# Optimization experiments

Measured on AMD Instinct MI355X. Metric: run time of the kernel, lower is better.

Reference implementation:

```python
import math
import jax, jax.numpy as jnp
from jax import lax
import numpy as np

B, S, D = 4, 128, 256          # batch, image side (l_max = S*S), d_model
FO = 64                        # filter_order (MLP width)
EMB = 3                        # emb_dim (time + 1 band sine/cosine)
FAST, SLOW, TARGET = 0.3, 1.5, 0.01


def setup_inputs() -> dict:
    key = jax.random.key(0)
    ks = jax.random.split(key, 20)
    d3 = 3 * D
    def rn(k, shp, scale):
        return jax.random.normal(k, shp, jnp.float32) * scale
    inp = {
        "x": jax.random.normal(ks[0], (B, S * S, D), jnp.float32),
        # in_proj / out_proj
        "in_w": rn(ks[1], (D, d3), 1.0 / math.sqrt(D)),
        "in_b": jnp.zeros((d3,), jnp.float32),
        "out_w": rn(ks[2], (D, D), 1.0 / math.sqrt(D)),
        "out_b": jnp.zeros((D,), jnp.float32),
        # depthwise 3x3 short filter
        "sf_w": rn(ks[3], (d3, 1, 3, 3), 1.0 / 3.0),
        "sf_b": jnp.zeros((d3,), jnp.float32),
        # Sin activation frequency (shared across all Sin uses; w=1, train_freq=True)
        "freq": jnp.ones((1, FO), jnp.float32),
        # X implicit filter MLP: Linear(3,FO) -> Sin -> Linear(FO,FO) -> Sin -> Linear(FO,FO) -> Sin -> Linear(FO,D,no bias)
        "xw0": rn(ks[4], (EMB, FO), 0.5), "xb0": jnp.zeros((FO,), jnp.float32),
        "xw1": rn(ks[5], (FO, FO), 1.0 / math.sqrt(FO)), "xb1": jnp.zeros((FO,), jnp.float32),
        "xw2": rn(ks[6], (FO, FO), 1.0 / math.sqrt(FO)), "xb2": jnp.zeros((FO,), jnp.float32),
        "xw3": rn(ks[7], (FO, D), 1.0 / math.sqrt(FO)),
        # Y implicit filter MLP (same structure)
        "yw0": rn(ks[8], (EMB, FO), 0.5), "yb0": jnp.zeros((FO,), jnp.float32),
        "yw1": rn(ks[9], (FO, FO), 1.0 / math.sqrt(FO)), "yb1": jnp.zeros((FO,), jnp.float32),
        "yw2": rn(ks[10], (FO, FO), 1.0 / math.sqrt(FO)), "yb2": jnp.zeros((FO,), jnp.float32),
        "yw3": rn(ks[11], (FO, D), 1.0 / math.sqrt(FO)),
        # HyenaFilter2d residual bias D (torch: randn)
        "fbias": jax.random.normal(ks[12], (D,), jnp.float32),
    }
    return inp


def _pos_emb():
    # PositionalEmbedding with emb_dim=3 -> bands=1
    t = jnp.linspace(0.0, 1.0, S)[None, :, None]                 # (1,S,1)
    tr = jnp.linspace(0.0, S - 1.0, S)[None, :, None]
    w_ang = 2.0 * math.pi * tr / S
    f = jnp.linspace(1e-4, 0.0, 1)[None, None]                   # bands=1
    zc = jnp.exp(-1j * f * w_ang)                                # (1,S,1) complex
    z = jnp.concatenate([t, zc.real, zc.imag], axis=-1)          # (1,S,3)
    return z.astype(jnp.float32), t.astype(jnp.float32)


def _decay(t):
    max_d = math.log(TARGET) / FAST
    min_d = math.log(TARGET) / SLOW
    deltas = jnp.linspace(min_d, max_d, D)[None, None]           # (1,1,D) buffer
    return jnp.exp(-t * jnp.abs(deltas))                         # (1,S,D)


def _mlp(z, freq, w0, b0, w1, b1, w2, b2, w3):
    h = jnp.sin(freq * (z @ w0 + b0))
    h = jnp.sin(freq * (h @ w1 + b1))
    h = jnp.sin(freq * (h @ w2 + b2))
    return h @ w3                                                # (1,S,D)


def _fftconv2d(u, k, Db):
    # u: (B,D,S,S), k: (D,S,S), Db: (D,)
    n = 2 * S
    kf = jnp.fft.rfft2(k.astype(jnp.float32), s=(n, n)) / n
    uf = jnp.fft.rfft2(u.astype(jnp.float32), s=(n, n))
    y = jnp.fft.irfft2(uf * kf, s=(n, n))[..., :S, :S]
    return y + u * Db[None, :, None, None]


def reference(x, in_w, in_b, out_w, out_b, sf_w, sf_b, freq,
              xw0, xb0, xw1, xb1, xw2, xb2, xw3,
              yw0, yb0, yw1, yb1, yw2, yb2, yw3, fbias):
    d3 = 3 * D
    # projection and reshape to 2D grid: b (h w) c -> b c h w
    u = x @ in_w + in_b                                          # (B,L,3D)
    u = u.reshape(B, S, S, d3).transpose(0, 3, 1, 2)             # (B,3D,S,S)
    # depthwise 3x3 short filter, padding=2, crop to S (matches Conv padding=2 + [:S])
    uc = lax.conv_general_dilated(u, sf_w, (1, 1), ((2, 2), (2, 2)),
                                  feature_group_count=d3,
                                  dimension_numbers=("NCHW", "OIHW", "NCHW"))
    uc = uc[..., :S, :S] + sf_b[None, :, None, None]
    x0, x1, v = jnp.split(uc, 3, axis=1)                         # each (B,D,S,S)
    # implicit separable 2D filter
    z, t = _pos_emb()
    dec = _decay(t)
    hx = _mlp(z, freq, xw0, xb0, xw1, xb1, xw2, xb2, xw3) * dec  # (1,S,D)
    hy = _mlp(z, freq, yw0, yb0, yw1, yb1, yw2, yb2, yw3) * dec
    k = jnp.einsum('ijk,imk->ijmk', hx, hy)[0]                   # (S,S,D)
    k = jnp.transpose(k, (2, 0, 1))                              # (D,S,S)
    # hyena recurrence (order=2): single gated fft conv
    v = v * x1
    v = _fftconv2d(v, k, fbias)
    y = v * x0
    y = y.transpose(0, 2, 3, 1).reshape(B, S * S, D)             # b c h w -> b (h w) c
    return y @ out_w + out_b
```

## Files before the change

kernel.cpp:

```cpp
#include <hip/hip_runtime.h>
#include <hip/hip_bf16.h>

#define S_DIM 128
#define B_DIM 4
#define L_DIM (S_DIM * S_DIM)

typedef __bf16 bf16x8 __attribute__((ext_vector_type(8)));
typedef float f32x4 __attribute__((ext_vector_type(4)));

__device__ __forceinline__ float b2f(unsigned short u) {
    union { unsigned int i; float f; } v;
    v.i = ((unsigned int)u) << 16;
    return v.f;
}
__device__ __forceinline__ unsigned short f2b(float f) {
    union { float f; unsigned int i; } v;
    v.f = f;
    unsigned int x = v.i;
    return (unsigned short)((x + 0x7FFFu + ((x >> 16) & 1u)) >> 16);
}
__device__ __forceinline__ float ldx(const void* p, size_t i, int f32) {
    return f32 ? ((const float*)p)[i] : b2f(((const unsigned short*)p)[i]);
}

__global__ __launch_bounds__(256) void sniff_dtype(const unsigned short* __restrict__ x,
                                                   int* __restrict__ flag) {
    __shared__ int cnt;
    if (threadIdx.x == 0) cnt = 0;
    __syncthreads();
    int c = 0;
    for (int i = threadIdx.x; i < 32768; i += 256) {
        unsigned int e = (x[i] >> 7) & 0xFFu;
        if (e >= 0x91u) c++;
    }
    atomicAdd(&cnt, c);
    __syncthreads();
    if (threadIdx.x == 0) flag[0] = (cnt > 64) ? 1 : 0;
}

__global__ void transpose_any(const void* __restrict__ src,
                              unsigned short* __restrict__ dst, int R, int C,
                              const int* __restrict__ flag) {
    const int f = flag[0];
    int idx = blockIdx.x * 256 + threadIdx.x;
    if (idx >= R * C) return;
    int r = idx / C, c = idx - r * C;
    dst[c * R + r] = f2b(ldx(src, idx, f));
}

__global__ __launch_bounds__(256) void filter_mlp(
    const void* __restrict__ freq,
    const void* __restrict__ w0, const void* __restrict__ b0,
    const void* __restrict__ w1, const void* __restrict__ b1,
    const void* __restrict__ w2, const void* __restrict__ b2,
    const void* __restrict__ w3,
    float* __restrict__ out, const int* __restrict__ flag)
{
    __shared__ float hs[64], gs[64];
    const int f32f = flag[0];
    const int s   = blockIdx.x;
    const int tid = threadIdx.x;
    const float t = (float)s / (float)(S_DIM - 1);
    const float ang = 1e-4f * 2.0f * 3.14159265358979323846f * ((float)s / (float)S_DIM);
    const float z0 = t, z1 = cosf(ang), z2 = -sinf(ang);

    if (tid < 64) {
        float fr = ldx(freq, tid, f32f);
        float a = z0 * ldx(w0, 0 * 64 + tid, f32f) + z1 * ldx(w0, 1 * 64 + tid, f32f) +
                  z2 * ldx(w0, 2 * 64 + tid, f32f) + ldx(b0, tid, f32f);
        hs[tid] = sinf(fr * a);
    }
    __syncthreads();
    if (tid < 64) {
        float fr = ldx(freq, tid, f32f);
        float a = ldx(b1, tid, f32f);
        for (int e = 0; e < 64; e++) a += hs[e] * ldx(w1, e * 64 + tid, f32f);
        gs[tid] = sinf(fr * a);
    }
    __syncthreads();
    if (tid < 64) {
        float fr = ldx(freq, tid, f32f);
        float a = ldx(b2, tid, f32f);
        for (int e = 0; e < 64; e++) a += gs[e] * ldx(w2, e * 64 + tid, f32f);
        hs[tid] = sinf(fr * a);
    }
    __syncthreads();
    {
        const float min_d = -3.0701134573253943f;
        const float max_d = -15.350567286626971f;
        float a = 0.f;
        for (int e = 0; e < 64; e++) a += hs[e] * ldx(w3, e * 256 + tid, f32f);
        float delta = min_d + (max_d - min_d) * ((float)tid / 255.0f);
        float dec = expf(-t * fabsf(delta));
        out[s * 256 + tid] = a * dec;
    }
}

__global__ __launch_bounds__(256) void gemm_bt(
    const void* __restrict__ A, size_t a_off, int a_ext,
    const unsigned short* __restrict__ BT,
    const void* __restrict__ bias, int bias_ext,
    void* __restrict__ C, size_t c_off, int c_ext,
    int M, int N, int K, const int* __restrict__ flag)
{
    __shared__ unsigned short As[128 * 40];
    __shared__ unsigned short Bs[128 * 40];

    const int f     = flag[0];
    const int a_f32 = a_ext && f;
    const int b_f32 = bias_ext && f;
    const int c_f32 = c_ext && f;

    const int tid  = threadIdx.x;
    const int m0   = blockIdx.x * 128;
    const int n0   = blockIdx.y * 128;
    const int wid  = tid >> 6;
    const int lane = tid & 63;
    const int lrow = lane & 15;
    const int quad = lane >> 4;
    const int wr   = wid >> 1, wc = wid & 1;

    f32x4 acc[4][4];
#pragma unroll
    for (int a = 0; a < 4; a++)
#pragma unroll
        for (int b = 0; b < 4; b++)
#pragma unroll
            for (int r = 0; r < 4; r++) acc[a][b][r] = 0.0f;

    for (int kc = 0; kc < K; kc += 32) {
#pragma unroll
        for (int h = 0; h < 2; h++) {
            int c    = tid + h * 256;
            int row  = c >> 2;
            int col8 = (c & 3) * 8;
            size_t aidx = a_off + (size_t)(m0 + row) * K + kc + col8;
            if (a_f32) {
                const float4* ga = (const float4*)((const float*)A + aidx);
                float4 p0 = ga[0], p1 = ga[1];
                uint4 w;
                w.x = (unsigned int)f2b(p0.x) | ((unsigned int)f2b(p0.y) << 16);
                w.y = (unsigned int)f2b(p0.z) | ((unsigned int)f2b(p0.w) << 16);
                w.z = (unsigned int)f2b(p1.x) | ((unsigned int)f2b(p1.y) << 16);
                w.w = (unsigned int)f2b(p1.z) | ((unsigned int)f2b(p1.w) << 16);
                *(uint4*)(&As[row * 40 + col8]) = w;
            } else {
                *(uint4*)(&As[row * 40 + col8]) =
                    *(const uint4*)((const unsigned short*)A + aidx);
            }
            *(uint4*)(&Bs[row * 40 + col8]) =
                *(const uint4*)(BT + (size_t)(n0 + row) * K + kc + col8);
        }
        __syncthreads();

        bf16x8 af[4], bfr[4];
#pragma unroll
        for (int fm = 0; fm < 4; fm++)
            af[fm] = *(const bf16x8*)(&As[(wr * 64 + fm * 16 + lrow) * 40 + quad * 8]);
#pragma unroll
        for (int fn = 0; fn < 4; fn++)
            bfr[fn] = *(const bf16x8*)(&Bs[(wc * 64 + fn * 16 + lrow) * 40 + quad * 8]);
#pragma unroll
        for (int fm = 0; fm < 4; fm++)
#pragma unroll
            for (int fn = 0; fn < 4; fn++)
                acc[fm][fn] = __builtin_amdgcn_mfma_f32_16x16x32_bf16(
                    af[fm], bfr[fn], acc[fm][fn], 0, 0, 0);
        __syncthreads();
    }

#pragma unroll
    for (int fm = 0; fm < 4; fm++) {
#pragma unroll
        for (int fn = 0; fn < 4; fn++) {
            int gcol = n0 + wc * 64 + fn * 16 + lrow;
            float bv = ldx(bias, gcol, b_f32);
#pragma unroll
            for (int r = 0; r < 4; r++) {
                int grow = m0 + wr * 64 + fm * 16 + quad * 4 + r;
                size_t cidx = c_off + (size_t)grow * N + gcol;
                float val = acc[fm][fn][r] + bv;
                if (c_f32) ((float*)C)[cidx] = val;
                else       ((unsigned short*)C)[cidx] = f2b(val);
            }
        }
    }
}

__global__ __launch_bounds__(192) void conv3_gate(
    const unsigned short* __restrict__ U, size_t u_zs,
    const void* __restrict__ sfw, const void* __restrict__ sfb,
    unsigned short* __restrict__ Wb, unsigned short* __restrict__ X0, size_t o_zs,
    const int* __restrict__ flag)
{
    __shared__ __align__(16) float x1f[2][256];

    const int f32f = flag[0];
    const int i    = blockIdx.x;
    const int j0   = blockIdx.y * 32;
    const int tid  = threadIdx.x;
    const int wv   = tid >> 6;
    const int lane = tid & 63;
    const int ch0  = wv * 256 + lane * 4;

    const unsigned short* Ub = U + (size_t)blockIdx.z * u_zs;
    unsigned short* Wbb = Wb + (size_t)blockIdx.z * o_zs;
    unsigned short* X0b = X0 + (size_t)blockIdx.z * o_zs;

    float wgt[3][3][4], bias[4];
#pragma unroll
    for (int c = 0; c < 4; c++) {
        int ch = ch0 + c;
        bias[c] = ldx(sfb, ch, f32f);
#pragma unroll
        for (int ki = 0; ki < 3; ki++)
#pragma unroll
            for (int kj = 0; kj < 3; kj++)
                wgt[ki][kj][c] = ldx(sfw, ch * 9 + ki * 3 + kj, f32f);
    }

    bool rok[3];
    const unsigned short* rp[3];
#pragma unroll
    for (int ki = 0; ki < 3; ki++) {
        int row = i + ki - 2;
        rok[ki] = (row >= 0);
        rp[ki]  = Ub + (size_t)(row * S_DIM) * 768 + ch0;
    }

    float win[3][3][4];
#define DLOAD(slot, col)                                                       \
    { _Pragma("unroll") for (int ki = 0; ki < 3; ki++) {                       \
        if (rok[ki] && (col) >= 0) {                                           \
            uint2 p = *(const uint2*)(rp[ki] + (size_t)(col) * 768);           \
            win[slot][ki][0] = b2f((unsigned short)p.x);                       \
            win[slot][ki][1] = b2f((unsigned short)(p.x >> 16));               \
            win[slot][ki][2] = b2f((unsigned short)p.y);                       \
            win[slot][ki][3] = b2f((unsigned short)(p.y >> 16));               \
        } else {                                                               \
            win[slot][ki][0] = 0.f; win[slot][ki][1] = 0.f;                    \
            win[slot][ki][2] = 0.f; win[slot][ki][3] = 0.f;                    \
        } } }

    DLOAD(0, j0 - 2)
    DLOAD(1, j0 - 1)

    uint2 nxt[3];
#pragma unroll
    for (int ki = 0; ki < 3; ki++) {
        uint2 p; p.x = 0u; p.y = 0u;
        if (rok[ki]) p = *(const uint2*)(rp[ki] + (size_t)j0 * 768);
        nxt[ki] = p;
    }

#pragma unroll
    for (int jj = 0; jj < 32; jj++) {
        const int j  = j0 + jj;
        const int sA = jj % 3, sB = (jj + 1) % 3, sC = (jj + 2) % 3;

#pragma unroll
        for (int ki = 0; ki < 3; ki++) {
            win[sC][ki][0] = b2f((unsigned short)nxt[ki].x);
            win[sC][ki][1] = b2f((unsigned short)(nxt[ki].x >> 16));
            win[sC][ki][2] = b2f((unsigned short)nxt[ki].y);
            win[sC][ki][3] = b2f((unsigned short)(nxt[ki].y >> 16));
        }
        {
            const int jn = j + 1;
            const bool jok = (jn < S_DIM);
#pragma unroll
            for (int ki = 0; ki < 3; ki++) {
                uint2 p; p.x = 0u; p.y = 0u;
                if (jok && rok[ki]) p = *(const uint2*)(rp[ki] + (size_t)jn * 768);
                nxt[ki] = p;
            }
        }

        float o[4];
#pragma unroll
        for (int c = 0; c < 4; c++) {
            float a = bias[c];
#pragma unroll
            for (int ki = 0; ki < 3; ki++)
                a += wgt[ki][0][c] * win[sA][ki][c]
                   + wgt[ki][1][c] * win[sB][ki][c]
                   + wgt[ki][2][c] * win[sC][ki][c];
            o[c] = a;
        }

        const size_t oidx = (size_t)(i * S_DIM + j) * 256 + lane * 4;
        if (wv == 1) {
            float4 v4; v4.x = o[0]; v4.y = o[1]; v4.z = o[2]; v4.w = o[3];
            *(float4*)(&x1f[jj & 1][lane * 4]) = v4;
        } else if (wv == 0) {
            unsigned int lo = (unsigned int)f2b(o[0]) | ((unsigned int)f2b(o[1]) << 16);
            unsigned int hi = (unsigned int)f2b(o[2]) | ((unsigned int)f2b(o[3]) << 16);
            uint2 st; st.x = lo; st.y = hi;
            *(uint2*)(&X0b[oidx]) = st;
        }
        __syncthreads();
        if (wv == 2) {
            float4 xp = *(const float4*)(&x1f[jj & 1][lane * 4]);
            float r0 = o[0] * xp.x;
            float r1 = o[1] * xp.y;
            float r2 = o[2] * xp.z;
            float r3 = o[3] * xp.w;
            unsigned int lo = (unsigned int)f2b(r0) | ((unsigned int)f2b(r1) << 16);
            unsigned int hi = (unsigned int)f2b(r2) | ((unsigned int)f2b(r3) << 16);
            uint2 st; st.x = lo; st.y = hi;
            *(uint2*)(&Wbb[oidx]) = st;
        }
    }
#undef DLOAD
}

__global__ __launch_bounds__(256) void conv_j(
    const unsigned short* __restrict__ Wb, size_t zs,
    const float* __restrict__ hy,
    unsigned short* __restrict__ Aout)
{
    __shared__ unsigned short wl[S_DIM * 256];
    const int i = blockIdx.x;
    const int h = blockIdx.y;
    const int tid = threadIdx.x;
    const size_t zoff = (size_t)blockIdx.z * zs;
    const size_t sbase = zoff + (size_t)(i * S_DIM) * 256;

    const uint4* gsrc = (const uint4*)(Wb + sbase);
    for (int c = tid; c < 4096; c += 256) ((uint4*)wl)[c] = gsrc[c];
    __syncthreads();

    const int d = tid;
    for (int pick = 0; pick < 2; pick++) {
        const int jt = pick ? (7 - h) : h;
        const int j0 = jt * 16;
        float acc[16];
#pragma unroll
        for (int jj = 0; jj < 16; jj++) acc[jj] = 0.f;

        float Wn[19];
#pragma unroll
        for (int t = 0; t < 19; t++) {
            int r = j0 - 3 + t;
            Wn[t] = (r >= 0) ? b2f(wl[r * 256 + d]) : 0.f;
        }
        const int qmax = j0 + 15;
        for (int q0 = 0; q0 <= qmax; q0 += 4) {
            float hv[4];
#pragma unroll
            for (int idx = 0; idx < 4; idx++) hv[idx] = hy[(q0 + idx) * 256 + d];
#pragma unroll
            for (int idx = 0; idx < 4; idx++)
#pragma unroll
                for (int jj = 0; jj < 16; jj++)
                    acc[jj] += hv[idx] * Wn[jj + 3 - idx];
            if (q0 + 4 <= qmax) {
#pragma unroll
                for (int t = 18; t >= 4; t--) Wn[t] = Wn[t - 4];
#pragma unroll
                for (int t = 0; t < 4; t++) {
                    int r = j0 - q0 - 7 + t;
                    Wn[t] = (r >= 0) ? b2f(wl[r * 256 + d]) : 0.f;
                }
            }
        }
#pragma unroll
        for (int jj = 0; jj < 16; jj++)
            Aout[sbase + (size_t)(j0 + jj) * 256 + d] = f2b(acc[jj]);
    }
}

__global__ __launch_bounds__(256) void conv_i(
    const unsigned short* __restrict__ Ain, size_t zs,
    const float* __restrict__ hx,
    const unsigned short* __restrict__ Wb,
    const unsigned short* __restrict__ X0,
    const void* __restrict__ fbias,
    unsigned short* __restrict__ Gout,
    const int* __restrict__ flag)
{
    __shared__ unsigned short al[S_DIM * 256];
    const int f32f = flag[0];
    const int j = blockIdx.x;
    const int h = blockIdx.y;
    const int tid = threadIdx.x;
    const size_t zoff = (size_t)blockIdx.z * zs;

    for (int c = tid; c < 4096; c += 256) {
        int row = c >> 5;
        int off = c & 31;
        const uint4* gsrc = (const uint4*)(Ain + zoff + (size_t)(row * S_DIM + j) * 256) + off;
        ((uint4*)al)[c] = *gsrc;
    }
    __syncthreads();

    const int d = tid;
    const float fb = ldx(fbias, d, f32f);
    for (int pick = 0; pick < 2; pick++) {
        const int it = pick ? (7 - h) : h;
        const int i0 = it * 16;
        float acc[16];
#pragma unroll
        for (int ii = 0; ii < 16; ii++) acc[ii] = 0.f;

        float Wn[19];
#pragma unroll
        for (int t = 0; t < 19; t++) {
            int r = i0 - 3 + t;
            Wn[t] = (r >= 0) ? b2f(al[r * 256 + d]) : 0.f;
        }
        const int qmax = i0 + 15;
        for (int q0 = 0; q0 <= qmax; q0 += 4) {
            float hv[4];
#pragma unroll
            for (int idx = 0; idx < 4; idx++) hv[idx] = hx[(q0 + idx) * 256 + d];
#pragma unroll
            for (int idx = 0; idx < 4; idx++)
#pragma unroll
                for (int ii = 0; ii < 16; ii++)
                    acc[ii] += hv[idx] * Wn[ii + 3 - idx];
            if (q0 + 4 <= qmax) {
#pragma unroll
                for (int t = 18; t >= 4; t--) Wn[t] = Wn[t - 4];
#pragma unroll
                for (int t = 0; t < 4; t++) {
                    int r = i0 - q0 - 7 + t;
                    Wn[t] = (r >= 0) ? b2f(al[r * 256 + d]) : 0.f;
                }
            }
        }
#pragma unroll
        for (int ii = 0; ii < 16; ii++) {
            int i = i0 + ii;
            size_t idx = zoff + (size_t)(i * S_DIM + j) * 256 + d;
            float wv  = b2f(Wb[idx]);
            float x0v = b2f(X0[idx]);
            float y = acc[ii] * (1.0f / 256.0f) + wv * fb;
            Gout[idx] = f2b(y * x0v);
        }
    }
}

extern "C" void kernel_launch(void* const* d_in, const int* in_sizes, int n_in,
                              void* d_out, int out_size, void* d_ws, size_t ws_size,
                              hipStream_t stream)
{
    const void* x     = d_in[0];
    const void* in_w  = d_in[1];
    const void* in_b  = d_in[2];
    const void* out_w = d_in[3];
    const void* out_b_= d_in[4];
    const void* sf_w  = d_in[5];
    const void* sf_b  = d_in[6];
    const void* freq  = d_in[7];
    const void* xw0 = d_in[8];  const void* xb0 = d_in[9];
    const void* xw1 = d_in[10]; const void* xb1 = d_in[11];
    const void* xw2 = d_in[12]; const void* xb2 = d_in[13];
    const void* xw3 = d_in[14];
    const void* yw0 = d_in[15]; const void* yb0 = d_in[16];
    const void* yw1 = d_in[17]; const void* yb1 = d_in[18];
    const void* yw2 = d_in[19]; const void* yb2 = d_in[20];
    const void* yw3 = d_in[21];
    const void* fbias = d_in[22];

    char* ws = (char*)d_ws;
    const size_t UZ  = (size_t)L_DIM * 768;
    const size_t OZ  = (size_t)L_DIM * 256;

    const size_t need_fused = 168558608;
    bool fused = (ws_size >= need_fused);

    if (fused) {
        unsigned short* u_f  = (unsigned short*)(ws + 0);
        unsigned short* A_f  = (unsigned short*)(ws + 0);
        unsigned short* G_f  = (unsigned short*)(ws + 33554432);
        unsigned short* Wb_f = (unsigned short*)(ws + 100663296);
        unsigned short* X0_f = (unsigned short*)(ws + 134217728);
        float* hx            = (float*)(ws + 167772160);
        float* hy            = (float*)(ws + 167903232);
        unsigned short* tin  = (unsigned short*)(ws + 168034304);
        unsigned short* tout = (unsigned short*)(ws + 168427520);
        int* flag            = (int*)(ws + 168558592);

        sniff_dtype<<<1, 256, 0, stream>>>((const unsigned short*)x, flag);
        transpose_any<<<dim3(768), 256, 0, stream>>>(in_w, tin, 256, 768, flag);
        transpose_any<<<dim3(256), 256, 0, stream>>>(out_w, tout, 256, 256, flag);
        filter_mlp<<<dim3(S_DIM), 256, 0, stream>>>(freq, xw0, xb0, xw1, xb1, xw2, xb2, xw3, hx, flag);
        filter_mlp<<<dim3(S_DIM), 256, 0, stream>>>(freq, yw0, yb0, yw1, yb1, yw2, yb2, yw3, hy, flag);

        gemm_bt<<<dim3(512, 6), 256, 0, stream>>>(
            x, 0, 1, tin, in_b, 1, u_f, 0, 0, B_DIM * L_DIM, 768, 256, flag);
        conv3_gate<<<dim3(S_DIM, 4, B_DIM), 192, 0, stream>>>(
            u_f, UZ, sf_w, sf_b, Wb_f, X0_f, OZ, flag);
        conv_j<<<dim3(S_DIM, 4, B_DIM), 256, 0, stream>>>(Wb_f, OZ, hy, A_f);
        conv_i<<<dim3(S_DIM, 4, B_DIM), 256, 0, stream>>>(
            A_f, OZ, hx, Wb_f, X0_f, fbias, G_f, flag);
        gemm_bt<<<dim3(512, 2), 256, 0, stream>>>(
            G_f, 0, 0, tout, out_b_, 1, d_out, 0, 1, B_DIM * L_DIM, 256, 256, flag);
    } else {
        unsigned short* u_b  = (unsigned short*)(ws + 0);
        unsigned short* A_b  = (unsigned short*)(ws + 0);
        unsigned short* G_b  = (unsigned short*)(ws + 8388608);
        unsigned short* Wb_b = (unsigned short*)(ws + 25165824);
        unsigned short* X0_b = (unsigned short*)(ws + 33554432);
        float* hx            = (float*)(ws + 41943040);
        float* hy            = (float*)(ws + 42074112);
        unsigned short* tin  = (unsigned short*)(ws + 42205184);
        unsigned short* tout = (unsigned short*)(ws + 42598400);
        int* flag            = (int*)(ws + 42729472);

        sniff_dtype<<<1, 256, 0, stream>>>((const unsigned short*)x, flag);
        transpose_any<<<dim3(768), 256, 0, stream>>>(in_w, tin, 256, 768, flag);
        transpose_any<<<dim3(256), 256, 0, stream>>>(out_w, tout, 256, 256, flag);
        filter_mlp<<<dim3(S_DIM), 256, 0, stream>>>(freq, xw0, xb0, xw1, xb1, xw2, xb2, xw3, hx, flag);
        filter_mlp<<<dim3(S_DIM), 256, 0, stream>>>(freq, yw0, yb0, yw1, yb1, yw2, yb2, yw3, hy, flag);

        for (int b = 0; b < B_DIM; b++) {
            size_t xoff = (size_t)b * OZ;
            gemm_bt<<<dim3(128, 6), 256, 0, stream>>>(
                x, xoff, 1, tin, in_b, 1, u_b, 0, 0, L_DIM, 768, 256, flag);
            conv3_gate<<<dim3(S_DIM, 4, 1), 192, 0, stream>>>(
                u_b, 0, sf_w, sf_b, Wb_b, X0_b, 0, flag);
            conv_j<<<dim3(S_DIM, 4, 1), 256, 0, stream>>>(Wb_b, 0, hy, A_b);
            conv_i<<<dim3(S_DIM, 4, 1), 256, 0, stream>>>(
                A_b, 0, hx, Wb_b, X0_b, fbias, G_b, flag);
            gemm_bt<<<dim3(128, 2), 256, 0, stream>>>(
                G_b, 0, 0, tout, out_b_, 1, d_out, xoff, 1, L_DIM, 256, 256, flag);
        }
    }
}
```

Before: 582.9 us.

## Fully unroll causal conv loops with ring-buffer window, one block per row, pre-cast x

The causal direct convolutions now have each block process all 8 output tiles of a row. The loops are fully unrolled and use a 20-slot register ring buffer indexed at compile time, which removes the per-step register shifting, and launch bounds request 2 blocks per CU. This cuts the grid fourfold so the shared-memory row is staged once instead of four times. A separate cast kernel converts x to bf16 before the input GEMM, so the GEMM reads bf16. The trade-offs are far fewer blocks (512) and lower parallelism for the conv kernels, a large unrolled code size, and an extra pass over x.

```diff
diff --git a/kernel.cpp b/kernel.cpp
--- a/kernel.cpp
+++ b/kernel.cpp
@@ -22,6 +22,8 @@
 __device__ __forceinline__ float ldx(const void* p, size_t i, int f32) {
     return f32 ? ((const float*)p)[i] : b2f(((const unsigned short*)p)[i]);
 }
+
+#define SLOT(r) ((((r) % 20) + 20) % 20)
 
 __global__ __launch_bounds__(256) void sniff_dtype(const unsigned short* __restrict__ x,
                                                    int* __restrict__ flag) {
@@ -46,6 +48,31 @@
     if (idx >= R * C) return;
     int r = idx / C, c = idx - r * C;
     dst[c * R + r] = f2b(ldx(src, idx, f));
+}
+
+__global__ __launch_bounds__(256) void cast_to_bf16(
+    const void* __restrict__ src, size_t s_off,
+    unsigned short* __restrict__ dst, size_t n,
+    const int* __restrict__ flag)
+{
+    const int f = flag[0];
+    size_t idx = ((size_t)blockIdx.x * 256 + threadIdx.x) * 8;
+    const size_t stride = (size_t)gridDim.x * 256 * 8;
+    for (; idx < n; idx += stride) {
+        if (f) {
+            const float4* s4 = (const float4*)((const float*)src + s_off + idx);
+            float4 a = s4[0], b = s4[1];
+            uint4 w;
+            w.x = (unsigned int)f2b(a.x) | ((unsigned int)f2b(a.y) << 16);
+            w.y = (unsigned int)f2b(a.z) | ((unsigned int)f2b(a.w) << 16);
+            w.z = (unsigned int)f2b(b.x) | ((unsigned int)f2b(b.y) << 16);
+            w.w = (unsigned int)f2b(b.z) | ((unsigned int)f2b(b.w) << 16);
+            *(uint4*)(dst + idx) = w;
+        } else {
+            *(uint4*)(dst + idx) =
+                *(const uint4*)((const unsigned short*)src + s_off + idx);
+        }
+    }
 }
 
 __global__ __launch_bounds__(256) void filter_mlp(
@@ -314,14 +341,13 @@
 #undef DLOAD
 }
 
-__global__ __launch_bounds__(256) void conv_j(
+__global__ __launch_bounds__(256, 2) void conv_j(
     const unsigned short* __restrict__ Wb, size_t zs,
     const float* __restrict__ hy,
     unsigned short* __restrict__ Aout)
 {
     __shared__ unsigned short wl[S_DIM * 256];
     const int i = blockIdx.x;
-    const int h = blockIdx.y;
     const int tid = threadIdx.x;
     const size_t zoff = (size_t)blockIdx.z * zs;
     const size_t sbase = zoff + (size_t)(i * S_DIM) * 256;
@@ -331,21 +357,24 @@
     __syncthreads();
 
     const int d = tid;
-    for (int pick = 0; pick < 2; pick++) {
-        const int jt = pick ? (7 - h) : h;
+    float win[20];
+
+#pragma unroll
+    for (int jt = 0; jt < 8; jt++) {
         const int j0 = jt * 16;
         float acc[16];
 #pragma unroll
         for (int jj = 0; jj < 16; jj++) acc[jj] = 0.f;
 
-        float Wn[19];
 #pragma unroll
         for (int t = 0; t < 19; t++) {
-            int r = j0 - 3 + t;
-            Wn[t] = (r >= 0) ? b2f(wl[r * 256 + d]) : 0.f;
-        }
-        const int qmax = j0 + 15;
-        for (int q0 = 0; q0 <= qmax; q0 += 4) {
+            const int r = j0 - 3 + t;
+            win[SLOT(r)] = (r >= 0) ? b2f(wl[r * 256 + d]) : 0.f;
+        }
+        const int nsteps = 4 * (jt + 1);
+#pragma unroll
+        for (int s = 0; s < nsteps; s++) {
+            const int q0 = 4 * s;
             float hv[4];
 #pragma unroll
             for (int idx = 0; idx < 4; idx++) hv[idx] = hy[(q0 + idx) * 256 + d];
@@ -353,14 +382,12 @@
             for (int idx = 0; idx < 4; idx++)
 #pragma unroll
                 for (int jj = 0; jj < 16; jj++)
-                    acc[jj] += hv[idx] * Wn[jj + 3 - idx];
-            if (q0 + 4 <= qmax) {
-#pragma unroll
-                for (int t = 18; t >= 4; t--) Wn[t] = Wn[t - 4];
+                    acc[jj] += hv[idx] * win[SLOT(j0 + jj - (q0 + idx))];
+            if (s + 1 < nsteps) {
 #pragma unroll
                 for (int t = 0; t < 4; t++) {
-                    int r = j0 - q0 - 7 + t;
-                    Wn[t] = (r >= 0) ? b2f(wl[r * 256 + d]) : 0.f;
+                    const int r = j0 - q0 - 7 + t;
+                    win[SLOT(r)] = (r >= 0) ? b2f(wl[r * 256 + d]) : 0.f;
                 }
             }
         }
@@ -370,7 +397,7 @@
     }
 }
 
-__global__ __launch_bounds__(256) void conv_i(
+__global__ __launch_bounds__(256, 2) void conv_i(
     const unsigned short* __restrict__ Ain, size_t zs,
     const float* __restrict__ hx,
     const unsigned short* __restrict__ Wb,
@@ -382,7 +409,6 @@
     __shared__ unsigned short al[S_DIM * 256];
     const int f32f = flag[0];
     const int j = blockIdx.x;
-    const int h = blockIdx.y;
     const int tid = threadIdx.x;
     const size_t zoff = (size_t)blockIdx.z * zs;
 
@@ -396,21 +422,24 @@
 
     const int d = tid;
     const float fb = ldx(fbias, d, f32f);
-    for (int pick = 0; pick < 2; pick++) {
-        const int it = pick ? (7 - h) : h;
+    float win[20];
+
+#pragma unroll
+    for (int it = 0; it < 8; it++) {
         const int i0 = it * 16;
         float acc[16];
 #pragma unroll
         for (int ii = 0; ii < 16; ii++) acc[ii] = 0.f;
 
-        float Wn[19];
 #pragma unroll
         for (int t = 0; t < 19; t++) {
-            int r = i0 - 3 + t;
-            Wn[t] = (r >= 0) ? b2f(al[r * 256 + d]) : 0.f;
-        }
-        const int qmax = i0 + 15;
-        for (int q0 = 0; q0 <= qmax; q0 += 4) {
+            const int r = i0 - 3 + t;
+            win[SLOT(r)] = (r >= 0) ? b2f(al[r * 256 + d]) : 0.f;
+        }
+        const int nsteps = 4 * (it + 1);
+#pragma unroll
+        for (int s = 0; s < nsteps; s++) {
+            const int q0 = 4 * s;
             float hv[4];
 #pragma unroll
             for (int idx = 0; idx < 4; idx++) hv[idx] = hx[(q0 + idx) * 256 + d];
@@ -418,14 +447,12 @@
             for (int idx = 0; idx < 4; idx++)
 #pragma unroll
                 for (int ii = 0; ii < 16; ii++)
-                    acc[ii] += hv[idx] * Wn[ii + 3 - idx];
-            if (q0 + 4 <= qmax) {
-#pragma unroll
-                for (int t = 18; t >= 4; t--) Wn[t] = Wn[t - 4];
+                    acc[ii] += hv[idx] * win[SLOT(i0 + ii - (q0 + idx))];
+            if (s + 1 < nsteps) {
 #pragma unroll
                 for (int t = 0; t < 4; t++) {
-                    int r = i0 - q0 - 7 + t;
-                    Wn[t] = (r >= 0) ? b2f(al[r * 256 + d]) : 0.f;
+                    const int r = i0 - q0 - 7 + t;
+                    win[SLOT(r)] = (r >= 0) ? b2f(al[r * 256 + d]) : 0.f;
                 }
             }
         }
@@ -476,6 +503,7 @@
         unsigned short* G_f  = (unsigned short*)(ws + 33554432);
         unsigned short* Wb_f = (unsigned short*)(ws + 100663296);
         unsigned short* X0_f = (unsigned short*)(ws + 134217728);
+        unsigned short* xb_f = (unsigned short*)(ws + 100663296);
         float* hx            = (float*)(ws + 167772160);
         float* hy            = (float*)(ws + 167903232);
         unsigned short* tin  = (unsigned short*)(ws + 168034304);
@@ -488,12 +516,14 @@
         filter_mlp<<<dim3(S_DIM), 256, 0, stream>>>(freq, xw0, xb0, xw1, xb1, xw2, xb2, xw3, hx, flag);
         filter_mlp<<<dim3(S_DIM), 256, 0, stream>>>(freq, yw0, yb0, yw1, yb1, yw2, yb2, yw3, hy, flag);
 
+        cast_to_bf16<<<dim3(2048), 256, 0, stream>>>(
+            x, 0, xb_f, (size_t)B_DIM * L_DIM * 256, flag);
         gemm_bt<<<dim3(512, 6), 256, 0, stream>>>(
-            x, 0, 1, tin, in_b, 1, u_f, 0, 0, B_DIM * L_DIM, 768, 256, flag);
+            xb_f, 0, 0, tin, in_b, 1, u_f, 0, 0, B_DIM * L_DIM, 768, 256, flag);
         conv3_gate<<<dim3(S_DIM, 4, B_DIM), 192, 0, stream>>>(
             u_f, UZ, sf_w, sf_b, Wb_f, X0_f, OZ, flag);
-        conv_j<<<dim3(S_DIM, 4, B_DIM), 256, 0, stream>>>(Wb_f, OZ, hy, A_f);
-        conv_i<<<dim3(S_DIM, 4, B_DIM), 256, 0, stream>>>(
+        conv_j<<<dim3(S_DIM, 1, B_DIM), 256, 0, stream>>>(Wb_f, OZ, hy, A_f);
+        conv_i<<<dim3(S_DIM, 1, B_DIM), 256, 0, stream>>>(
             A_f, OZ, hx, Wb_f, X0_f, fbias, G_f, flag);
         gemm_bt<<<dim3(512, 2), 256, 0, stream>>>(
             G_f, 0, 0, tout, out_b_, 1, d_out, 0, 1, B_DIM * L_DIM, 256, 256, flag);
@@ -503,6 +533,7 @@
         unsigned short* G_b  = (unsigned short*)(ws + 8388608);
         unsigned short* Wb_b = (unsigned short*)(ws + 25165824);
         unsigned short* X0_b = (unsigned short*)(ws + 33554432);
+        unsigned short* xb_b = (unsigned short*)(ws + 25165824);
         float* hx            = (float*)(ws + 41943040);
         float* hy            = (float*)(ws + 42074112);
         unsigned short* tin  = (unsigned short*)(ws + 42205184);
@@ -517,12 +548,14 @@
 
         for (int b = 0; b < B_DIM; b++) {
             size_t xoff = (size_t)b * OZ;
+            cast_to_bf16<<<dim3(2048), 256, 0, stream>>>(
+                x, xoff, xb_b, (size_t)L_DIM * 256, flag);
             gemm_bt<<<dim3(128, 6), 256, 0, stream>>>(
-                x, xoff, 1, tin, in_b, 1, u_b, 0, 0, L_DIM, 768, 256, flag);
+                xb_b, 0, 0, tin, in_b, 1, u_b, 0, 0, L_DIM, 768, 256, flag);
             conv3_gate<<<dim3(S_DIM, 4, 1), 192, 0, stream>>>(
                 u_b, 0, sf_w, sf_b, Wb_b, X0_b, 0, flag);
-            conv_j<<<dim3(S_DIM, 4, 1), 256, 0, stream>>>(Wb_b, 0, hy, A_b);
-            conv_i<<<dim3(S_DIM, 4, 1), 256, 0, stream>>>(
+            conv_j<<<dim3(S_DIM, 1, 1), 256, 0, stream>>>(Wb_b, 0, hy, A_b);
+            conv_i<<<dim3(S_DIM, 1, 1), 256, 0, stream>>>(
                 A_b, 0, hx, Wb_b, X0_b, fbias, G_b, flag);
             gemm_bt<<<dim3(128, 2), 256, 0, stream>>>(
                 G_b, 0, 0, tout, out_b_, 1, d_out, xoff, 1, L_DIM, 256, 256, flag);
```

New measurement: 849.5 us. +45.7%, slower.

## Pre-cast input to bf16 and read conv operands directly from global memory

Applied to the files above, without the earlier changes.

Adds a separate pass that casts x to bf16 into the Wb workspace region before the input projection GEMM, so the GEMM reads bf16 instead of per-element converted input. conv_j and conv_i no longer stage a full 64KB row or column slab into LDS; they read the sliding window straight from global memory and double-buffer the filter-tap loads. This targets LDS occupancy limits and the staging barrier, at the cost of an extra cast pass and more scattered, strided global reads in conv_i.

```diff
diff --git a/kernel.cpp b/kernel.cpp
--- a/kernel.cpp
+++ b/kernel.cpp
@@ -46,6 +46,31 @@
     if (idx >= R * C) return;
     int r = idx / C, c = idx - r * C;
     dst[c * R + r] = f2b(ldx(src, idx, f));
+}
+
+__global__ __launch_bounds__(256) void cast_to_bf16(
+    const void* __restrict__ src, size_t s_off,
+    unsigned short* __restrict__ dst, size_t n,
+    const int* __restrict__ flag)
+{
+    const int f = flag[0];
+    size_t idx = ((size_t)blockIdx.x * 256 + threadIdx.x) * 8;
+    const size_t stride = (size_t)gridDim.x * 256 * 8;
+    for (; idx < n; idx += stride) {
+        if (f) {
+            const float4* s4 = (const float4*)((const float*)src + s_off + idx);
+            float4 a = s4[0], b = s4[1];
+            uint4 w;
+            w.x = (unsigned int)f2b(a.x) | ((unsigned int)f2b(a.y) << 16);
+            w.y = (unsigned int)f2b(a.z) | ((unsigned int)f2b(a.w) << 16);
+            w.z = (unsigned int)f2b(b.x) | ((unsigned int)f2b(b.y) << 16);
+            w.w = (unsigned int)f2b(b.z) | ((unsigned int)f2b(b.w) << 16);
+            *(uint4*)(dst + idx) = w;
+        } else {
+            *(uint4*)(dst + idx) =
+                *(const uint4*)((const unsigned short*)src + s_off + idx);
+        }
+    }
 }
 
 __global__ __launch_bounds__(256) void filter_mlp(
@@ -319,18 +344,14 @@
     const float* __restrict__ hy,
     unsigned short* __restrict__ Aout)
 {
-    __shared__ unsigned short wl[S_DIM * 256];
     const int i = blockIdx.x;
     const int h = blockIdx.y;
-    const int tid = threadIdx.x;
+    const int d = threadIdx.x;
     const size_t zoff = (size_t)blockIdx.z * zs;
     const size_t sbase = zoff + (size_t)(i * S_DIM) * 256;
-
-    const uint4* gsrc = (const uint4*)(Wb + sbase);
-    for (int c = tid; c < 4096; c += 256) ((uint4*)wl)[c] = gsrc[c];
-    __syncthreads();
-
-    const int d = tid;
+    const unsigned short* Wp = Wb + sbase + d;
+    const float* hyd = hy + d;
+
     for (int pick = 0; pick < 2; pick++) {
         const int jt = pick ? (7 - h) : h;
         const int j0 = jt * 16;
@@ -342,25 +363,44 @@
 #pragma unroll
         for (int t = 0; t < 19; t++) {
             int r = j0 - 3 + t;
-            Wn[t] = (r >= 0) ? b2f(wl[r * 256 + d]) : 0.f;
+            Wn[t] = (r >= 0) ? b2f(Wp[(size_t)r * 256]) : 0.f;
         }
         const int qmax = j0 + 15;
-        for (int q0 = 0; q0 <= qmax; q0 += 4) {
-            float hv[4];
-#pragma unroll
-            for (int idx = 0; idx < 4; idx++) hv[idx] = hy[(q0 + idx) * 256 + d];
+        float hvA[4], hvB[4];
+#pragma unroll
+        for (int idx = 0; idx < 4; idx++) hvA[idx] = hyd[idx * 256];
+
+        for (int q0 = 0; q0 <= qmax; q0 += 8) {
+#pragma unroll
+            for (int idx = 0; idx < 4; idx++) hvB[idx] = hyd[(q0 + 4 + idx) * 256];
 #pragma unroll
             for (int idx = 0; idx < 4; idx++)
 #pragma unroll
                 for (int jj = 0; jj < 16; jj++)
-                    acc[jj] += hv[idx] * Wn[jj + 3 - idx];
-            if (q0 + 4 <= qmax) {
+                    acc[jj] += hvA[idx] * Wn[jj + 3 - idx];
+#pragma unroll
+            for (int t = 18; t >= 4; t--) Wn[t] = Wn[t - 4];
+#pragma unroll
+            for (int t = 0; t < 4; t++) {
+                int r = j0 - q0 - 7 + t;
+                Wn[t] = (r >= 0) ? b2f(Wp[(size_t)r * 256]) : 0.f;
+            }
+            if (q0 + 8 <= qmax) {
+#pragma unroll
+                for (int idx = 0; idx < 4; idx++) hvA[idx] = hyd[(q0 + 8 + idx) * 256];
+            }
+#pragma unroll
+            for (int idx = 0; idx < 4; idx++)
+#pragma unroll
+                for (int jj = 0; jj < 16; jj++)
+                    acc[jj] += hvB[idx] * Wn[jj + 3 - idx];
+            if (q0 + 8 <= qmax) {
 #pragma unroll
                 for (int t = 18; t >= 4; t--) Wn[t] = Wn[t - 4];
 #pragma unroll
                 for (int t = 0; t < 4; t++) {
-                    int r = j0 - q0 - 7 + t;
-                    Wn[t] = (r >= 0) ? b2f(wl[r * 256 + d]) : 0.f;
+                    int r = j0 - q0 - 11 + t;
+                    Wn[t] = (r >= 0) ? b2f(Wp[(size_t)r * 256]) : 0.f;
                 }
             }
         }
@@ -379,23 +419,15 @@
     unsigned short* __restrict__ Gout,
     const int* __restrict__ flag)
 {
-    __shared__ unsigned short al[S_DIM * 256];
     const int f32f = flag[0];
     const int j = blockIdx.x;
     const int h = blockIdx.y;
-    const int tid = threadIdx.x;
+    const int d = threadIdx.x;
     const size_t zoff = (size_t)blockIdx.z * zs;
-
-    for (int c = tid; c < 4096; c += 256) {
-        int row = c >> 5;
-        int off = c & 31;
-        const uint4* gsrc = (const uint4*)(Ain + zoff + (size_t)(row * S_DIM + j) * 256) + off;
-        ((uint4*)al)[c] = *gsrc;
-    }
-    __syncthreads();
-
-    const int d = tid;
+    const unsigned short* Ap = Ain + zoff + (size_t)j * 256 + d;
+    const float* hxd = hx + d;
     const float fb = ldx(fbias, d, f32f);
+
     for (int pick = 0; pick < 2; pick++) {
         const int it = pick ? (7 - h) : h;
         const int i0 = it * 16;
@@ -407,25 +439,44 @@
 #pragma unroll
         for (int t = 0; t < 19; t++) {
             int r = i0 - 3 + t;
-            Wn[t] = (r >= 0) ? b2f(al[r * 256 + d]) : 0.f;
+            Wn[t] = (r >= 0) ? b2f(Ap[(size_t)r * (S_DIM * 256)]) : 0.f;
         }
         const int qmax = i0 + 15;
-        for (int q0 = 0; q0 <= qmax; q0 += 4) {
-            float hv[4];
-#pragma unroll
-            for (int idx = 0; idx < 4; idx++) hv[idx] = hx[(q0 + idx) * 256 + d];
+        float hvA[4], hvB[4];
+#pragma unroll
+        for (int idx = 0; idx < 4; idx++) hvA[idx] = hxd[idx * 256];
+
+        for (int q0 = 0; q0 <= qmax; q0 += 8) {
+#pragma unroll
+            for (int idx = 0; idx < 4; idx++) hvB[idx] = hxd[(q0 + 4 + idx) * 256];
 #pragma unroll
             for (int idx = 0; idx < 4; idx++)
 #pragma unroll
                 for (int ii = 0; ii < 16; ii++)
-                    acc[ii] += hv[idx] * Wn[ii + 3 - idx];
-            if (q0 + 4 <= qmax) {
+                    acc[ii] += hvA[idx] * Wn[ii + 3 - idx];
+#pragma unroll
+            for (int t = 18; t >= 4; t--) Wn[t] = Wn[t - 4];
+#pragma unroll
+            for (int t = 0; t < 4; t++) {
+                int r = i0 - q0 - 7 + t;
+                Wn[t] = (r >= 0) ? b2f(Ap[(size_t)r * (S_DIM * 256)]) : 0.f;
+            }
+            if (q0 + 8 <= qmax) {
+#pragma unroll
+                for (int idx = 0; idx < 4; idx++) hvA[idx] = hxd[(q0 + 8 + idx) * 256];
+            }
+#pragma unroll
+            for (int idx = 0; idx < 4; idx++)
+#pragma unroll
+                for (int ii = 0; ii < 16; ii++)
+                    acc[ii] += hvB[idx] * Wn[ii + 3 - idx];
+            if (q0 + 8 <= qmax) {
 #pragma unroll
                 for (int t = 18; t >= 4; t--) Wn[t] = Wn[t - 4];
 #pragma unroll
                 for (int t = 0; t < 4; t++) {
-                    int r = i0 - q0 - 7 + t;
-                    Wn[t] = (r >= 0) ? b2f(al[r * 256 + d]) : 0.f;
+                    int r = i0 - q0 - 11 + t;
+                    Wn[t] = (r >= 0) ? b2f(Ap[(size_t)r * (S_DIM * 256)]) : 0.f;
                 }
             }
         }
@@ -476,6 +527,7 @@
         unsigned short* G_f  = (unsigned short*)(ws + 33554432);
         unsigned short* Wb_f = (unsigned short*)(ws + 100663296);
         unsigned short* X0_f = (unsigned short*)(ws + 134217728);
+        unsigned short* xb_f = (unsigned short*)(ws + 100663296);
         float* hx            = (float*)(ws + 167772160);
         float* hy            = (float*)(ws + 167903232);
         unsigned short* tin  = (unsigned short*)(ws + 168034304);
@@ -488,8 +540,10 @@
         filter_mlp<<<dim3(S_DIM), 256, 0, stream>>>(freq, xw0, xb0, xw1, xb1, xw2, xb2, xw3, hx, flag);
         filter_mlp<<<dim3(S_DIM), 256, 0, stream>>>(freq, yw0, yb0, yw1, yb1, yw2, yb2, yw3, hy, flag);
 
+        cast_to_bf16<<<dim3(2048), 256, 0, stream>>>(
+            x, 0, xb_f, (size_t)B_DIM * L_DIM * 256, flag);
         gemm_bt<<<dim3(512, 6), 256, 0, stream>>>(
-            x, 0, 1, tin, in_b, 1, u_f, 0, 0, B_DIM * L_DIM, 768, 256, flag);
+            xb_f, 0, 0, tin, in_b, 1, u_f, 0, 0, B_DIM * L_DIM, 768, 256, flag);
         conv3_gate<<<dim3(S_DIM, 4, B_DIM), 192, 0, stream>>>(
             u_f, UZ, sf_w, sf_b, Wb_f, X0_f, OZ, flag);
         conv_j<<<dim3(S_DIM, 4, B_DIM), 256, 0, stream>>>(Wb_f, OZ, hy, A_f);
@@ -503,6 +557,7 @@
         unsigned short* G_b  = (unsigned short*)(ws + 8388608);
         unsigned short* Wb_b = (unsigned short*)(ws + 25165824);
         unsigned short* X0_b = (unsigned short*)(ws + 33554432);
+        unsigned short* xb_b = (unsigned short*)(ws + 25165824);
         float* hx            = (float*)(ws + 41943040);
         float* hy            = (float*)(ws + 42074112);
         unsigned short* tin  = (unsigned short*)(ws + 42205184);
@@ -517,8 +572,10 @@
 
         for (int b = 0; b < B_DIM; b++) {
             size_t xoff = (size_t)b * OZ;
+            cast_to_bf16<<<dim3(2048), 256, 0, stream>>>(
+                x, xoff, xb_b, (size_t)L_DIM * 256, flag);
             gemm_bt<<<dim3(128, 6), 256, 0, stream>>>(
-                x, xoff, 1, tin, in_b, 1, u_b, 0, 0, L_DIM, 768, 256, flag);
+                xb_b, 0, 0, tin, in_b, 1, u_b, 0, 0, L_DIM, 768, 256, flag);
             conv3_gate<<<dim3(S_DIM, 4, 1), 192, 0, stream>>>(
                 u_b, 0, sf_w, sf_b, Wb_b, X0_b, 0, flag);
             conv_j<<<dim3(S_DIM, 4, 1), 256, 0, stream>>>(Wb_b, 0, hy, A_b);
```

Result: slower. 603.7 us (+3.6%).
